# Kernel tuning notes

Measured on AMD Instinct MI355X. Metric: run time of the kernel, lower is better.

Reference implementation:

```python
import math
import jax, jax.numpy as jnp
import numpy as np

D_MODEL = 1024
N_HEAD = 16
HEAD_DIM = D_MODEL // N_HEAD  # 64
B = 8
L = 512
USE_GAUSSIAN = True
SCALE = 1.0  # scale=False in __init__


def rel_sin_pos_embed(seq_len, dim):
    # RelativeSinusoidalPositionalEmbedding: table row at index (pos+origin_shift)
    # holds [sin(pos*inv_freq), cos(pos*inv_freq)]; forward selects positions
    # arange(-L/2, round(L/2)) -> for even L this is -L/2 .. L/2-1.
    half = dim // 2
    inv_freq = jnp.exp(jnp.arange(half, dtype=jnp.float32) * (-math.log(10000.0) / (half - 1)))
    rel = jnp.arange(-(seq_len // 2), seq_len - seq_len // 2, dtype=jnp.float32)  # [L]
    ang = rel[:, None] * inv_freq[None, :]  # [L, half]
    return jnp.concatenate([jnp.sin(ang), jnp.cos(ang)], axis=-1)  # [L, dim]


def setup_inputs() -> dict:
    key = jax.random.key(0)
    ks = jax.random.split(key, 8)
    x = jax.random.normal(ks[0], (B, L, D_MODEL), dtype=jnp.float32)
    mask = jax.random.randint(ks[1], (B, L), 0, 2, dtype=jnp.int32)
    # guarantee at least one valid key per row so softmax never sees all -inf
    mask = mask.at[:, 0].set(1)
    qmask = jax.random.randint(ks[2], (B, L), 0, 2, dtype=jnp.int64)
    s = 0.02
    W_qkv = jax.random.normal(ks[3], (5 * D_MODEL, D_MODEL), dtype=jnp.float32) * s
    W_pos = jax.random.normal(ks[4], (3 * D_MODEL, HEAD_DIM), dtype=jnp.float32) * s
    W_fc = jax.random.normal(ks[5], (D_MODEL, D_MODEL), dtype=jnp.float32) * s
    b_fc = jnp.zeros((D_MODEL,), dtype=jnp.float32)
    # shift = abs(randn)+eps (positive), bias = -abs(randn); small scale keeps softmax sane
    shift = jnp.abs(jax.random.normal(ks[6], (1,), dtype=jnp.float32)) * 1e-4 + 1e-5
    bias = -jnp.abs(jax.random.normal(ks[7], (1,), dtype=jnp.float32))
    return {"x": x, "mask": mask, "qmask": qmask, "W_qkv": W_qkv, "W_pos": W_pos,
            "W_fc": W_fc, "b_fc": b_fc, "shift": shift, "bias": bias}


def reference(x, mask, qmask, W_qkv, W_pos, W_fc, b_fc, shift, bias):
    Bs, Ls, D = x.shape
    H, hd = N_HEAD, D // N_HEAD

    qkv = jnp.einsum('bld,ed->ble', x, W_qkv)  # [B, L, 5D]
    q, k, k1, k2, v = jnp.split(qkv, 5, axis=-1)

    def heads(t):  # [B, L, D] -> [B, H, L, hd]
        return t.reshape(Bs, Ls, H, hd).transpose(0, 2, 1, 3)

    q, k1, k2, v = heads(q), heads(k1), heads(k2), heads(v)

    pe = jax.lax.stop_gradient(rel_sin_pos_embed(Ls, hd))  # [L, hd], detached in torch
    y = jnp.einsum('ld,ed->le', pe, W_pos)  # [L, 3D]
    q_p, k1_p, k2_p = jnp.split(y, 3, axis=-1)
    q_p = q_p.reshape(Ls, H, hd).transpose(1, 0, 2)   # [H, L, hd]
    k1_p = k1_p.reshape(Ls, H, hd).transpose(1, 0, 2)  # [H, L, hd]
    k2_p = k2_p.reshape(Ls, H, hd).transpose(1, 0, 2)

    attn_self = jnp.einsum('bhid,bhjd->bhij', q, k1) + jnp.einsum('hid,hjd->hij', q_p, k1_p)[None]
    attn_others = jnp.einsum('bhid,bhjd->bhij', q, k2) + jnp.einsum('hid,hjd->hij', q_p, k2_p)[None]

    same = (qmask[:, :, None] == qmask[:, None, :])[:, None]  # [B, 1, L, L]
    attn = jnp.where(same, attn_self, 0.0) + jnp.where(same, 0.0, attn_others)
    attn = attn / SCALE
    attn = jnp.where(mask[:, None, None, :] == 0, -jnp.inf, attn)

    if USE_GAUSSIAN:
        idx = jnp.arange(Ls, dtype=jnp.float32)
        sq_dist = (idx[:, None] - idx[None, :]) ** 2  # [L, L]
        attn = attn + (-(shift[0] * sq_dist + bias[0]))[None, None]

    attn = jax.nn.softmax(attn, axis=-1)
    out = jnp.einsum('bhij,bhjd->bhid', attn, v)  # [B, H, L, hd]
    out = out.transpose(0, 2, 1, 3).reshape(Bs, Ls, D)
    return jnp.einsum('bld,ed->ble', out, W_fc) + b_fc
```

## Files before the change

### kernel.cpp

```cpp
#include <hip/hip_runtime.h>

#define DM 1024
#define HN 16
#define HD 64
#define BB 8
#define LL 512

typedef __bf16 bf16x8 __attribute__((ext_vector_type(8)));
typedef __bf16 bf16x4 __attribute__((ext_vector_type(4)));
typedef float  f32x4  __attribute__((ext_vector_type(4)));

__device__ __forceinline__ void cvt8(const float* __restrict__ in,
                                     __bf16* __restrict__ out, int i) {
    const float4* p = (const float4*)in + (size_t)i * 2;
    float4 a = p[0], b = p[1];
    bf16x8 v;
    v[0] = (__bf16)a.x; v[1] = (__bf16)a.y; v[2] = (__bf16)a.z; v[3] = (__bf16)a.w;
    v[4] = (__bf16)b.x; v[5] = (__bf16)b.y; v[6] = (__bf16)b.z; v[7] = (__bf16)b.w;
    ((bf16x8*)out)[i] = v;
}

__global__ __launch_bounds__(512) void prep_kernel(
    const int* __restrict__ qmask, const int* __restrict__ maskp,
    const float* __restrict__ x, const float* __restrict__ W_qkv,
    const float* __restrict__ W_pos, const float* __restrict__ W_fc,
    int* __restrict__ perm, int* __restrict__ pmask, float* __restrict__ posf,
    int* __restrict__ nzA, __bf16* __restrict__ PEb, __bf16* __restrict__ Wposb,
    __bf16* __restrict__ Wfcb, __bf16* __restrict__ Xb, __bf16* __restrict__ Wqkvb)
{
    const int blk = blockIdx.x, tid = threadIdx.x;
    if (blk < 8) {
        int b = blk, i = tid;
        int qm = qmask[b * LL + i];
        unsigned long long bz = __ballot(qm == 0);
        int wid = i >> 6, lane = i & 63;
        __shared__ int wz[8];
        int pzw = __popcll(bz & ((1ULL << lane) - 1ULL));
        if (lane == 0) wz[wid] = __popcll(bz);
        __syncthreads();
        int base = 0, nz = 0;
#pragma unroll
        for (int w2 = 0; w2 < 8; ++w2) { int c = wz[w2]; if (w2 < wid) base += c; nz += c; }
        int zbefore = base + pzw;
        int pos = (qm == 0) ? zbefore : (nz + (i - zbefore));
        perm[b * LL + pos] = i;
        pmask[b * LL + pos] = maskp[b * LL + i];
        posf[b * LL + pos] = (float)i;
        if (i == 0) nzA[b] = nz;
    } else if (blk < 72) {
        int idx = (blk - 8) * 512 + tid;
        int l = idx >> 6, d = idx & 63;
        float p = (float)(l - LL / 2);
        const float cexp = -9.210340371976184f / 31.0f;
        float val;
        if (d < 32) { float f = expf((float)d * cexp);        val = sinf(p * f); }
        else        { float f = expf((float)(d - 32) * cexp); val = cosf(p * f); }
        PEb[idx] = (__bf16)val;
    } else if (blk < 120) {
        cvt8(W_pos, Wposb, (blk - 72) * 512 + tid);
    } else if (blk < 376) {
        cvt8(W_fc, Wfcb, (blk - 120) * 512 + tid);
    } else if (blk < 1400) {
        cvt8(x, Xb, (blk - 376) * 512 + tid);
    } else if (blk < 1656) {
        cvt8(W_qkv, Wqkvb, (blk - 1400) * 512 + tid);
    } else {
        cvt8(W_qkv + 2097152, Wqkvb + 1048576, (blk - 1656) * 512 + tid);
    }
}

template<int MODE>
__global__ __launch_bounds__(256, 4) void gemm_mfma(
    const __bf16* __restrict__ A, const __bf16* __restrict__ Bm,
    __bf16* __restrict__ Qc, __bf16* __restrict__ K1c,
    __bf16* __restrict__ K2c, __bf16* __restrict__ Vn,
    float* __restrict__ outF, const float* __restrict__ bias, int K)
{
    __shared__ __bf16 smem[128 * 136];
    __bf16* As = smem;
    __bf16* Bs = smem + 8192;
    __bf16* Cs = smem;
    const int tid = threadIdx.x;
    const int lane = tid & 63;
    const int w = tid >> 6;
    const int wm = w >> 1, wn = w & 1;
    const int n0 = blockIdx.x * 128;
    const int m0 = blockIdx.y * 128;
    const int fr = lane & 15;
    const int fq = lane >> 4;

    const int srow = tid >> 3;
    const int scol = (tid & 7) ^ (srow & 7);
    const __bf16* Ag = A + (size_t)(m0 + srow) * K + scol * 8;
    const __bf16* Bg = Bm + (size_t)(n0 + srow) * K + scol * 8;
    char* AsB = (char*)As + (size_t)w * 1024;
    char* BsB = (char*)Bs + (size_t)w * 1024;

    f32x4 acc[4][4] = {};

    for (int k0 = 0; k0 < K; k0 += 64) {
#pragma unroll
        for (int r = 0; r < 4; ++r) {
            __builtin_amdgcn_global_load_lds(Ag + k0 + (size_t)(r * 32) * K, AsB + r * 4096, 16, 0, 0);
            __builtin_amdgcn_global_load_lds(Bg + k0 + (size_t)(r * 32) * K, BsB + r * 4096, 16, 0, 0);
        }
        __syncthreads();

#pragma unroll
        for (int kk = 0; kk < 2; ++kk) {
            const int so = ((kk * 4 + fq) ^ (fr & 7)) * 8;
            bf16x8 af[4], bfr[4];
#pragma unroll
            for (int i = 0; i < 4; ++i)
                af[i] = *(const bf16x8*)(As + (size_t)(wm * 64 + i * 16 + fr) * 64 + so);
#pragma unroll
            for (int j = 0; j < 4; ++j)
                bfr[j] = *(const bf16x8*)(Bs + (size_t)(wn * 64 + j * 16 + fr) * 64 + so);
#pragma unroll
            for (int i = 0; i < 4; ++i)
#pragma unroll
                for (int j = 0; j < 4; ++j)
                    acc[i][j] = __builtin_amdgcn_mfma_f32_16x16x32_bf16(bfr[j], af[i], acc[i][j], 0, 0, 0);
        }
        __syncthreads();
    }

    if constexpr (MODE == 0 || MODE == 2) {
#pragma unroll
        for (int i = 0; i < 4; ++i) {
            int mloc = wm * 64 + i * 16 + fr;
#pragma unroll
            for (int j = 0; j < 4; ++j) {
                int nloc = wn * 64 + j * 16 + fq * 4;
                bf16x4 v;
#pragma unroll
                for (int r = 0; r < 4; ++r) v[r] = (__bf16)acc[i][j][r];
                *(bf16x4*)(Cs + (size_t)mloc * 136 + nloc) = v;
            }
        }
        __syncthreads();
        if constexpr (MODE == 0) {
            const int c = n0 >> 10;
            __bf16* T = (c == 0) ? Qc : (c == 1) ? K1c : (c == 2) ? K2c : Vn;
            const int b = m0 >> 9, l0 = m0 & 511, h0 = (n0 >> 6) & 15;
#pragma unroll
            for (int rnd = 0; rnd < 8; ++rnd) {
                int Ci = rnd * 256 + tid;
                int m = Ci >> 4, nch = Ci & 15;
                bf16x8 v = *(const bf16x8*)(Cs + (size_t)m * 136 + nch * 8);
                int hl = nch >> 3, d = (nch & 7) * 8;
                size_t bh2 = (size_t)(b * HN + h0 + hl);
                if (c < 3) *(bf16x8*)(T + (bh2 * LL + l0 + m) * 128 + d) = v;
                else       *(bf16x8*)(T + (bh2 * LL + l0 + m) * 64  + d) = v;
            }
        } else {
            const int c = n0 >> 10;
            __bf16* T = (c == 0) ? Qc : (c == 1) ? K1c : K2c;
#pragma unroll
            for (int rnd = 0; rnd < 8; ++rnd) {
                int Ci = rnd * 256 + tid;
                int m = Ci >> 4, nch = Ci & 15;
                bf16x8 v = *(const bf16x8*)(Cs + (size_t)m * 136 + nch * 8);
                int eg = n0 + nch * 8;
                int h = (eg >> 6) & 15, d = eg & 63;
                size_t off = ((size_t)h * LL + (m0 + m)) * 128 + 64 + d;
#pragma unroll
                for (int b = 0; b < 8; ++b)
                    *(bf16x8*)(T + (size_t)b * (HN * LL * 128) + off) = v;
            }
        }
    } else {
#pragma unroll
        for (int i = 0; i < 4; ++i) {
            int m = m0 + wm * 64 + i * 16 + fr;
#pragma unroll
            for (int j = 0; j < 4; ++j) {
                int nn = n0 + wn * 64 + j * 16 + fq * 4;
                float4 bv = *(const float4*)(bias + nn);
                *(float4*)(outF + (size_t)m * DM + nn) =
                    make_float4(acc[i][j][0] + bv.x, acc[i][j][1] + bv.y,
                                acc[i][j][2] + bv.z, acc[i][j][3] + bv.w);
            }
        }
    }
}

__global__ __launch_bounds__(256) void vtrans_kernel(const __bf16* __restrict__ Vn,
                                                     const int* __restrict__ perm,
                                                     __bf16* __restrict__ Vt) {
    __shared__ __bf16 Ts[64][72];
    int bh = blockIdx.x >> 3, lt = blockIdx.x & 7;
    int b = bh >> 4;
    int r = threadIdx.x >> 2, s = threadIdx.x & 3;
    int orow = perm[b * LL + lt * 64 + r];
    const __bf16* src = Vn + ((size_t)bh * LL + orow) * 64;
    *(bf16x8*)&Ts[r][s * 16]     = *(const bf16x8*)(src + s * 16);
    *(bf16x8*)&Ts[r][s * 16 + 8] = *(const bf16x8*)(src + s * 16 + 8);
    __syncthreads();
    __bf16* dst = Vt + ((size_t)bh * 64 + r) * LL + lt * 64 + s * 16;
    bf16x8 a, bvv;
#pragma unroll
    for (int e = 0; e < 8; ++e) { a[e] = Ts[s * 16 + e][r]; bvv[e] = Ts[s * 16 + 8 + e][r]; }
    *(bf16x8*)dst = a;
    *(bf16x8*)(dst + 8) = bvv;
}

__global__ __launch_bounds__(512, 2) void attn_kernel(
    const __bf16* __restrict__ Qc, const __bf16* __restrict__ K1c,
    const __bf16* __restrict__ K2c, const __bf16* __restrict__ Vt,
    const int* __restrict__ pmask, const int* __restrict__ perm,
    const float* __restrict__ posf, const int* __restrict__ nzA,
    const float* __restrict__ shiftp, const float* __restrict__ biasp,
    __bf16* __restrict__ AO)
{
    __shared__ __bf16 Ke0[64 * 136];
    __shared__ __bf16 Ke1[64 * 136];
    __shared__ __bf16 Vts[64 * 88];
    __shared__ __bf16 Sb[8 * 16 * 72];
    __shared__ __align__(16) float posL[64];

    const int tid = threadIdx.x;
    const int lane = tid & 63;
    const int wid = tid >> 6;
    const int fr = lane & 15;
    const int fq = lane >> 4;

    const int bid = (blockIdx.x & 7) * 64 + (blockIdx.x >> 3);
    const int qt = bid & 3;
    const int h  = (bid >> 2) & 15;
    const int b  = bid >> 6;
    const size_t bh = (size_t)(b * HN + h);
    const int nz = nzA[b];
    const int q0blk = qt * 128;
    const int s = q0blk + wid * 16 + fr;
    const int pi = perm[b * LL + s];
    const bool need0 = (q0blk < nz);
    const bool need1 = (q0blk + 127 >= nz);
    const int w0 = q0blk + wid * 16;
    const bool wneed0 = (w0 < nz);
    const bool wneed1 = (w0 + 15 >= nz);
    const int qmI = (s >= nz) ? 1 : 0;

    const float sft = shiftp[0];

    bf16x8 qf[4];
    {
        const __bf16* qrow = Qc + (bh * LL + pi) * 128;
#pragma unroll
        for (int kf = 0; kf < 4; ++kf)
            qf[kf] = *(const bf16x8*)(qrow + kf * 32 + fq * 8);
    }

    float mrun = -1e30f, lrun = 0.f;
    f32x4 ot[4] = {};
    const float qposf = (float)pi;

    const __bf16* K1g0 = K1c + bh * LL * 128;
    const __bf16* K2g0 = K2c + bh * LL * 128;
    const __bf16* Vtg0 = Vt + bh * 64 * LL;
    __bf16* Sw = Sb + wid * 16 * 72;

    const int krr = tid >> 4;
    const int ku  = tid & 15;
    const int vrr = tid >> 3;
    const int vu  = tid & 7;

    bf16x8 rk0[2], rk1[2], rv;
    int pm; float ppos;

#define LOAD_TILE(tt)                                                              \
    {                                                                              \
        int j0_ = (tt) * 64;                                                       \
        _Pragma("unroll")                                                          \
        for (int p = 0; p < 2; ++p) {                                              \
            int sr = j0_ + p * 32 + krr;                                           \
            int orow = perm[b * LL + sr];                                          \
            int qmj = (sr >= nz) ? 1 : 0;                                          \
            const __bf16* s1 = (qmj ? K2g0 : K1g0) + (size_t)orow * 128 + ku * 8;  \
            const __bf16* s2 = (qmj ? K1g0 : K2g0) + (size_t)orow * 128 + ku * 8;  \
            if (need0) rk0[p] = *(const bf16x8*)s1;                                \
            if (need1) rk1[p] = *(const bf16x8*)s2;                                \
        }                                                                          \
        rv = *(const bf16x8*)(Vtg0 + (size_t)vrr * LL + j0_ + vu * 8);             \
        pm = pmask[b * LL + j0_ + lane];                                           \
        ppos = posf[b * LL + j0_ + lane];                                          \
    }

    LOAD_TILE(0);

    for (int t = 0; t < 8; ++t) {
        __syncthreads();
        {
#pragma unroll
            for (int p = 0; p < 2; ++p) {
                int rr = p * 32 + krr;
                if (need0) *(bf16x8*)(Ke0 + rr * 136 + ku * 8) = rk0[p];
                if (need1) *(bf16x8*)(Ke1 + rr * 136 + ku * 8) = rk1[p];
            }
            *(bf16x8*)(Vts + vrr * 88 + vu * 8) = rv;
            if (wid == 0) posL[lane] = ppos;
        }
        unsigned long long kbits = __ballot(pm != 0);
        if (t < 7) LOAD_TILE(t + 1);
        __syncthreads();

        f32x4 acc[4];
        if (wneed0 != wneed1) {
            const __bf16* Ks = wneed0 ? Ke0 : Ke1;
            __builtin_amdgcn_s_setprio(1);
#pragma unroll
            for (int kb = 0; kb < 4; ++kb) {
                bf16x8 af[4];
#pragma unroll
                for (int kf = 0; kf < 4; ++kf)
                    af[kf] = *(const bf16x8*)(Ks + (kb * 16 + fr) * 136 + kf * 32 + fq * 8);
                f32x4 a = {};
#pragma unroll
                for (int kf = 0; kf < 4; ++kf)
                    a = __builtin_amdgcn_mfma_f32_16x16x32_bf16(af[kf], qf[kf], a, 0, 0, 0);
                acc[kb] = a;
            }
            __builtin_amdgcn_s_setprio(0);
        } else {
            __builtin_amdgcn_s_setprio(1);
#pragma unroll
            for (int kb = 0; kb < 4; ++kb) {
                bf16x8 a0f[4], a1f[4];
#pragma unroll
                for (int kf = 0; kf < 4; ++kf) {
                    a0f[kf] = *(const bf16x8*)(Ke0 + (kb * 16 + fr) * 136 + kf * 32 + fq * 8);
                    a1f[kf] = *(const bf16x8*)(Ke1 + (kb * 16 + fr) * 136 + kf * 32 + fq * 8);
                }
                f32x4 t0 = {}, t1 = {};
#pragma unroll
                for (int kf = 0; kf < 4; ++kf) {
                    t0 = __builtin_amdgcn_mfma_f32_16x16x32_bf16(a0f[kf], qf[kf], t0, 0, 0, 0);
                    t1 = __builtin_amdgcn_mfma_f32_16x16x32_bf16(a1f[kf], qf[kf], t1, 0, 0, 0);
                }
#pragma unroll
                for (int r = 0; r < 4; ++r) acc[kb][r] = qmI ? t1[r] : t0[r];
            }
            __builtin_amdgcn_s_setprio(0);
        }

#pragma unroll
        for (int kb = 0; kb < 4; ++kb) {
            f32x4 pj = *(const f32x4*)(posL + kb * 16 + fq * 4);
#pragma unroll
            for (int r = 0; r < 4; ++r) {
                int ko = kb * 16 + fq * 4 + r;
                float di = qposf - pj[r];
                float v = acc[kb][r] - sft * di * di;
                acc[kb][r] = ((int)(kbits >> ko) & 1) ? v : -1e30f;
            }
        }

        float mn = mrun;
#pragma unroll
        for (int kb = 0; kb < 4; ++kb)
#pragma unroll
            for (int r = 0; r < 4; ++r) mn = fmaxf(mn, acc[kb][r]);
        mn = fmaxf(mn, __shfl_xor(mn, 16));
        mn = fmaxf(mn, __shfl_xor(mn, 32));
        float sc = __expf(mrun - mn);
        mrun = mn;
        float sum = 0.f;
#pragma unroll
        for (int kb = 0; kb < 4; ++kb)
#pragma unroll
            for (int r = 0; r < 4; ++r) {
                float p = __expf(acc[kb][r] - mn);
                acc[kb][r] = p;
                sum += p;
            }
        sum += __shfl_xor(sum, 16);
        sum += __shfl_xor(sum, 32);
        lrun = lrun * sc + sum;
#pragma unroll
        for (int fd = 0; fd < 4; ++fd)
#pragma unroll
            for (int r = 0; r < 4; ++r) ot[fd][r] *= sc;

#pragma unroll
        for (int kb = 0; kb < 4; ++kb) {
            bf16x4 pk;
#pragma unroll
            for (int r = 0; r < 4; ++r) pk[r] = (__bf16)acc[kb][r];
            *(bf16x4*)(Sw + fr * 72 + kb * 16 + fq * 4) = pk;
        }
        bf16x8 pf0 = *(const bf16x8*)(Sw + fr * 72 + fq * 8);
        bf16x8 pf1 = *(const bf16x8*)(Sw + fr * 72 + 32 + fq * 8);
        __builtin_amdgcn_s_setprio(1);
#pragma unroll
        for (int fd = 0; fd < 4; ++fd) {
            bf16x8 v0 = *(const bf16x8*)(Vts + (fd * 16 + fr) * 88 + fq * 8);
            bf16x8 v1 = *(const bf16x8*)(Vts + (fd * 16 + fr) * 88 + 32 + fq * 8);
            ot[fd] = __builtin_amdgcn_mfma_f32_16x16x32_bf16(v0, pf0, ot[fd], 0, 0, 0);
            ot[fd] = __builtin_amdgcn_mfma_f32_16x16x32_bf16(v1, pf1, ot[fd], 0, 0, 0);
        }
        __builtin_amdgcn_s_setprio(0);
    }
#undef LOAD_TILE

    {
        const float inv = 1.0f / lrun;
#pragma unroll
        for (int fd = 0; fd < 4; ++fd) {
            bf16x4 o;
#pragma unroll
            for (int r = 0; r < 4; ++r) o[r] = (__bf16)(ot[fd][r] * inv);
            *(bf16x4*)(Sw + fr * 72 + fd * 16 + fq * 4) = o;
        }
    }
    __syncthreads();
    {
        int r = tid >> 2, c = tid & 3;
        int pir = perm[b * LL + q0blk + r];
        const __bf16* src = Sb + (r >> 4) * (16 * 72) + (r & 15) * 72;
        __bf16* dst = AO + ((size_t)(b * LL + pir)) * DM + h * 64;
        *(bf16x8*)(dst + c * 8)      = *(const bf16x8*)(src + c * 8);
        *(bf16x8*)(dst + 32 + c * 8) = *(const bf16x8*)(src + 32 + c * 8);
    }
}

extern "C" void kernel_launch(void* const* d_in, const int* in_sizes, int n_in,
                              void* d_out, int out_size, void* d_ws, size_t ws_size,
                              hipStream_t stream) {
    const float* x     = (const float*)d_in[0];
    const int*   mask  = (const int*)d_in[1];
    const int*   qmask = (const int*)d_in[2];
    const float* W_qkv = (const float*)d_in[3];
    const float* W_pos = (const float*)d_in[4];
    const float* W_fc  = (const float*)d_in[5];
    const float* b_fc  = (const float*)d_in[6];
    const float* shift = (const float*)d_in[7];
    const float* bias  = (const float*)d_in[8];
    float* out = (float*)d_out;

    __bf16* Qcb  = (__bf16*)d_ws;
    __bf16* K1cb = Qcb  + 8388608;
    __bf16* K2cb = K1cb + 8388608;
    __bf16* Vnb  = K2cb + 8388608;
    __bf16* Vtb  = Vnb  + 4194304;
    __bf16* Xb   = Vtb  + 4194304;
    __bf16* Wqkvb = Xb  + 4194304;
    __bf16* AOb   = Xb;
    __bf16* PEb   = Wqkvb + 4194304;
    __bf16* Wposb = PEb + 32768;
    __bf16* Wfcb  = Wposb + 196608;
    int* permA = (int*)(Wfcb + 1048576);
    int* nzA   = permA + 4096;
    int* pmaskA = nzA + 8;
    float* posfA = (float*)(pmaskA + 4096);

    prep_kernel<<<2424, 512, 0, stream>>>(qmask, mask, x, W_qkv, W_pos, W_fc,
                                          permA, pmaskA, posfA, nzA,
                                          PEb, Wposb, Wfcb, Xb, Wqkvb);
    gemm_mfma<0><<<dim3(32, 32), 256, 0, stream>>>(Xb, Wqkvb, Qcb, K1cb, K2cb, Vnb,
                                                   nullptr, nullptr, 1024);
    vtrans_kernel<<<1024, 256, 0, stream>>>(Vnb, permA, Vtb);
    gemm_mfma<2><<<dim3(24, 4), 256, 0, stream>>>(PEb, Wposb, Qcb, K1cb, K2cb, nullptr,
                                                  nullptr, nullptr, 64);
    attn_kernel<<<512, 512, 0, stream>>>(Qcb, K1cb, K2cb, Vtb, pmaskA, permA,
                                         posfA, nzA, shift, bias, AOb);
    gemm_mfma<1><<<dim3(8, 32), 256, 0, stream>>>(AOb, Wfcb, nullptr, nullptr, nullptr,
                                                  nullptr, out, b_fc, 1024);
}
```

Baseline: 131.2 us.

## Load V tiles directly to registers and add lazy softmax rescaling

Removes shared-memory staging of V^T and position values; each wave loads its V fragments and positions directly from global memory into registers. Online softmax skips the max update and accumulator rescale when the tile max stays within a threshold of the running max, and masked keys contribute zero directly. This cuts LDS traffic and exp/rescale work, but raises register pressure and redundant global/L2 reads across waves.

```diff
diff --git a/kernel.cpp b/kernel.cpp
--- a/kernel.cpp
+++ b/kernel.cpp
@@ -215,9 +215,7 @@
 {
     __shared__ __bf16 Ke0[64 * 136];
     __shared__ __bf16 Ke1[64 * 136];
-    __shared__ __bf16 Vts[64 * 88];
     __shared__ __bf16 Sb[8 * 16 * 72];
-    __shared__ __align__(16) float posL[64];
 
     const int tid = threadIdx.x;
     const int lane = tid & 63;
@@ -258,15 +256,14 @@
     const __bf16* K1g0 = K1c + bh * LL * 128;
     const __bf16* K2g0 = K2c + bh * LL * 128;
     const __bf16* Vtg0 = Vt + bh * 64 * LL;
+    const float* posg = posf + b * LL;
     __bf16* Sw = Sb + wid * 16 * 72;
 
     const int krr = tid >> 4;
     const int ku  = tid & 15;
-    const int vrr = tid >> 3;
-    const int vu  = tid & 7;
-
-    bf16x8 rk0[2], rk1[2], rv;
-    int pm; float ppos;
+
+    bf16x8 rk0[2], rk1[2];
+    int pm;
 
 #define LOAD_TILE(tt)                                                              \
     {                                                                              \
@@ -281,14 +278,13 @@
             if (need0) rk0[p] = *(const bf16x8*)s1;                                \
             if (need1) rk1[p] = *(const bf16x8*)s2;                                \
         }                                                                          \
-        rv = *(const bf16x8*)(Vtg0 + (size_t)vrr * LL + j0_ + vu * 8);             \
         pm = pmask[b * LL + j0_ + lane];                                           \
-        ppos = posf[b * LL + j0_ + lane];                                          \
     }
 
     LOAD_TILE(0);
 
     for (int t = 0; t < 8; ++t) {
+        const int j0 = t * 64;
         __syncthreads();
         {
 #pragma unroll
@@ -297,11 +293,15 @@
                 if (need0) *(bf16x8*)(Ke0 + rr * 136 + ku * 8) = rk0[p];
                 if (need1) *(bf16x8*)(Ke1 + rr * 136 + ku * 8) = rk1[p];
             }
-            *(bf16x8*)(Vts + vrr * 88 + vu * 8) = rv;
-            if (wid == 0) posL[lane] = ppos;
         }
         unsigned long long kbits = __ballot(pm != 0);
         if (t < 7) LOAD_TILE(t + 1);
+        bf16x8 vtf[4][2];
+#pragma unroll
+        for (int fd = 0; fd < 4; ++fd)
+#pragma unroll
+            for (int hf = 0; hf < 2; ++hf)
+                vtf[fd][hf] = *(const bf16x8*)(Vtg0 + (size_t)(fd * 16 + fr) * LL + j0 + hf * 32 + fq * 8);
         __syncthreads();
 
         f32x4 acc[4];
@@ -345,41 +345,44 @@
 
 #pragma unroll
         for (int kb = 0; kb < 4; ++kb) {
-            f32x4 pj = *(const f32x4*)(posL + kb * 16 + fq * 4);
+            f32x4 pj = *(const f32x4*)(posg + j0 + kb * 16 + fq * 4);
+#pragma unroll
+            for (int r = 0; r < 4; ++r) {
+                float di = qposf - pj[r];
+                acc[kb][r] -= sft * di * di;
+            }
+        }
+
+        float lmax = acc[0][0];
+#pragma unroll
+        for (int kb = 0; kb < 4; ++kb)
+#pragma unroll
+            for (int r = 0; r < 4; ++r) lmax = fmaxf(lmax, acc[kb][r]);
+        if (!__all(lmax <= mrun + 8.f)) {
+            float mn = fmaxf(mrun, lmax);
+            mn = fmaxf(mn, __shfl_xor(mn, 16));
+            mn = fmaxf(mn, __shfl_xor(mn, 32));
+            float sc = __expf(mrun - mn);
+            mrun = mn;
+            lrun *= sc;
+#pragma unroll
+            for (int fd = 0; fd < 4; ++fd)
+#pragma unroll
+                for (int r = 0; r < 4; ++r) ot[fd][r] *= sc;
+        }
+        float sum = 0.f;
+#pragma unroll
+        for (int kb = 0; kb < 4; ++kb)
 #pragma unroll
             for (int r = 0; r < 4; ++r) {
                 int ko = kb * 16 + fq * 4 + r;
-                float di = qposf - pj[r];
-                float v = acc[kb][r] - sft * di * di;
-                acc[kb][r] = ((int)(kbits >> ko) & 1) ? v : -1e30f;
-            }
-        }
-
-        float mn = mrun;
-#pragma unroll
-        for (int kb = 0; kb < 4; ++kb)
-#pragma unroll
-            for (int r = 0; r < 4; ++r) mn = fmaxf(mn, acc[kb][r]);
-        mn = fmaxf(mn, __shfl_xor(mn, 16));
-        mn = fmaxf(mn, __shfl_xor(mn, 32));
-        float sc = __expf(mrun - mn);
-        mrun = mn;
-        float sum = 0.f;
-#pragma unroll
-        for (int kb = 0; kb < 4; ++kb)
-#pragma unroll
-            for (int r = 0; r < 4; ++r) {
-                float p = __expf(acc[kb][r] - mn);
+                float p = ((int)(kbits >> ko) & 1) ? __expf(acc[kb][r] - mrun) : 0.f;
                 acc[kb][r] = p;
                 sum += p;
             }
         sum += __shfl_xor(sum, 16);
         sum += __shfl_xor(sum, 32);
-        lrun = lrun * sc + sum;
-#pragma unroll
-        for (int fd = 0; fd < 4; ++fd)
-#pragma unroll
-            for (int r = 0; r < 4; ++r) ot[fd][r] *= sc;
+        lrun += sum;
 
 #pragma unroll
         for (int kb = 0; kb < 4; ++kb) {
@@ -393,10 +396,8 @@
         __builtin_amdgcn_s_setprio(1);
 #pragma unroll
         for (int fd = 0; fd < 4; ++fd) {
-            bf16x8 v0 = *(const bf16x8*)(Vts + (fd * 16 + fr) * 88 + fq * 8);
-            bf16x8 v1 = *(const bf16x8*)(Vts + (fd * 16 + fr) * 88 + 32 + fq * 8);
-            ot[fd] = __builtin_amdgcn_mfma_f32_16x16x32_bf16(v0, pf0, ot[fd], 0, 0, 0);
-            ot[fd] = __builtin_amdgcn_mfma_f32_16x16x32_bf16(v1, pf1, ot[fd], 0, 0, 0);
+            ot[fd] = __builtin_amdgcn_mfma_f32_16x16x32_bf16(vtf[fd][0], pf0, ot[fd], 0, 0, 0);
+            ot[fd] = __builtin_amdgcn_mfma_f32_16x16x32_bf16(vtf[fd][1], pf1, ot[fd], 0, 0, 0);
         }
         __builtin_amdgcn_s_setprio(0);
     }
```

New measurement: 150.2 us. 14.5% more time.
